# Optimization experiments

Measured on AMD Instinct MI355X. Metric: run time of the kernel, lower is better.

## Reference

```python
import jax, jax.numpy as jnp
import numpy as np

B = 8192        # number of drug-cell pairs (graphs)
NPG = 32        # nodes per graph
EPG = 64        # directed edges per graph
N = B * NPG     # total nodes
E = B * EPG     # total edges
CELL = 908      # cell_inp_dim
BN_EPS = 1e-5


def _bn(x):
    # BatchNorm1d in training mode with gamma=1, beta=0 (fresh init), biased var
    m = x.mean(0)
    v = x.var(0)
    return (x - m) * jax.lax.rsqrt(v + BN_EPS)


def _lin_params(k, fan_in, fan_out):
    kw, _ = jax.random.split(k)
    w = jax.random.normal(kw, (fan_in, fan_out), jnp.float32) / np.sqrt(fan_in)
    b = jnp.zeros((fan_out,), jnp.float32)
    return w, b


_DIMS = [("ce_1", CELL, 516), ("ce_2", 516, 256), ("ce_3", 256, 128),
         ("g1_1", 9, 128), ("g1_2", 128, 128),
         ("g2_1", 128, 128), ("g2_2", 128, 128),
         ("d_1", 128, 128), ("d_2", 128, 128),
         ("f_1", 256, 128), ("f_2", 128, 64), ("f_3", 64, 1)]


def setup_inputs() -> dict:
    key = jax.random.key(0)
    ks = jax.random.split(key, 4 + len(_DIMS))
    inp = {}
    inp["cell"] = jax.random.normal(ks[0], (B, CELL), jnp.float32)
    inp["drug_x"] = jax.random.normal(ks[1], (N, 9), jnp.float32)
    g = jnp.arange(E) // EPG  # graph id per edge
    src = g * NPG + jax.random.randint(ks[2], (E,), 0, NPG)
    dst = g * NPG + jax.random.randint(ks[3], (E,), 0, NPG)
    inp["drug_edge_index"] = jnp.stack([src, dst]).astype(jnp.int32)
    inp["drug_batch"] = (jnp.arange(N) // NPG).astype(jnp.int32)
    for i, (nm, a, b) in enumerate(_DIMS):
        w, bb = _lin_params(ks[4 + i], a, b)
        inp[nm + "_w"] = w
        inp[nm + "_b"] = bb
    return inp


def _forward(cell, drug_x, src, dst, batch,
             ce_1_w, ce_1_b, ce_2_w, ce_2_b, ce_3_w, ce_3_b,
             g1_1_w, g1_1_b, g1_2_w, g1_2_b,
             g2_1_w, g2_1_b, g2_2_w, g2_2_b,
             d_1_w, d_1_b, d_2_w, d_2_b,
             f_1_w, f_1_b, f_2_w, f_2_b, f_3_w, f_3_b):
    # cell_emb branch (dropout = identity in eval/reference)
    c = jax.nn.relu(_bn(cell @ ce_1_w + ce_1_b))
    c = jax.nn.relu(_bn(c @ ce_2_w + ce_2_b))
    c = jax.nn.relu(_bn(c @ ce_3_w + ce_3_b))

    # GINConv 1: h = MLP((1+eps)*x + sum_{j in N(i)} x_j), eps=0
    agg = jax.ops.segment_sum(drug_x[src], dst, num_segments=N)
    h = drug_x + agg
    h = jax.nn.relu(_bn(h @ g1_1_w + g1_1_b)) @ g1_2_w + g1_2_b  # inner MLP: Lin-BN-ReLU-Lin
    h = _bn(jax.nn.relu(h))  # outer ReLU then BN (per Sequential order)

    # GINConv 2
    agg = jax.ops.segment_sum(h[src], dst, num_segments=N)
    h = h + agg
    h = jax.nn.relu(_bn(h @ g2_1_w + g2_1_b)) @ g2_2_w + g2_2_b
    h = _bn(jax.nn.relu(h))

    # global max pool over nodes of each graph -> [B, 128]
    p = jax.ops.segment_max(h, batch, num_segments=B)

    d = jax.nn.relu(_bn(p @ d_1_w + d_1_b))
    d = jax.nn.relu(d @ d_2_w + d_2_b)

    z = jnp.concatenate([c, d], axis=-1)  # [B, 256]
    z = jax.nn.elu(_bn(z @ f_1_w + f_1_b))
    z = jax.nn.elu(_bn(z @ f_2_w + f_2_b))
    y = (z @ f_3_w + f_3_b).reshape(B)
    return y


def reference(cell, drug_x, drug_edge_index, drug_batch,
              ce_1_w, ce_1_b, ce_2_w, ce_2_b, ce_3_w, ce_3_b,
              g1_1_w, g1_1_b, g1_2_w, g1_2_b,
              g2_1_w, g2_1_b, g2_2_w, g2_2_b,
              d_1_w, d_1_b, d_2_w, d_2_b,
              f_1_w, f_1_b, f_2_w, f_2_b, f_3_w, f_3_b):
    src, dst = drug_edge_index[0], drug_edge_index[1]
    return _forward(cell, drug_x, src, dst, drug_batch,
                    ce_1_w, ce_1_b, ce_2_w, ce_2_b, ce_3_w, ce_3_b,
                    g1_1_w, g1_1_b, g1_2_w, g1_2_b,
                    g2_1_w, g2_1_b, g2_2_w, g2_2_b,
                    d_1_w, d_1_b, d_2_w, d_2_b,
                    f_1_w, f_1_b, f_2_w, f_2_b, f_3_w, f_3_b)
```

## Files before the change

kernel.cpp:

```cpp
#include <hip/hip_runtime.h>
#include <hip/hip_bf16.h>
#include <math.h>

#define BGRAPH 8192
#define NPG 32
#define EPG 64
#define NNODE (BGRAPH * NPG)
#define NEDGE (BGRAPH * EPG)
#define CELLD 908
#define BN_EPS 1e-5f
#define ABF_STR 960
#define C1_STR 576

typedef __attribute__((ext_vector_type(8))) short bf16x8;
typedef __attribute__((ext_vector_type(4))) float f32x4;
typedef __attribute__((ext_vector_type(4))) unsigned short us4;
typedef __attribute__((ext_vector_type(8))) unsigned short us8;

__device__ __forceinline__ unsigned short f2bf(float f)
{
    unsigned int u = __float_as_uint(f);
    u = (u + 0x7FFFu + ((u >> 16) & 1u)) >> 16;
    return (unsigned short)u;
}

__device__ __forceinline__ bf16x8 quant8(const float v[8])
{
    union { bf16x8 b; unsigned short u[8]; } fr;
    #pragma unroll
    for (int j = 0; j < 8; ++j) fr.u[j] = f2bf(v[j]);
    return fr.b;
}

__device__ __forceinline__ void bf2f8(bf16x8 b, float v[8])
{
    union { bf16x8 bb; unsigned short u[8]; } x; x.bb = b;
    #pragma unroll
    for (int j = 0; j < 8; ++j) v[j] = __uint_as_float((unsigned)x.u[j] << 16);
}

__device__ __forceinline__ float apply_in(float v, int mode, float mn, float iv)
{
    if (mode == 1)      { v = (v - mn) * iv; v = fmaxf(v, 0.f); }
    else if (mode == 2) { v = (v - mn) * iv; v = (v > 0.f) ? v : expm1f(v); }
    else if (mode == 3) { v = fmaxf(v, 0.f); v = (v - mn) * iv; }
    return v;
}

struct TransArgs {
    const float* w[11];
    unsigned short* wt[11];
    int K[11], N[11], ntN[11];
    int off[12];
};

__global__ void transpose_w(TransArgs a)
{
    __shared__ float t[64][65];
    int b = blockIdx.x, tid = threadIdx.x;
    int s = 0;
    while (s < 10 && b >= a.off[s + 1]) ++s;
    int t0 = b - a.off[s];
    int K = a.K[s], N = a.N[s], ntn = a.ntN[s];
    int kt = t0 / ntn, nt = t0 - kt * ntn;
    int k0 = kt * 64, n0 = nt * 64;
    const float* w = a.w[s];
    unsigned short* wt = a.wt[s];
    int c = tid & 63, rg = tid >> 6;
    #pragma unroll
    for (int i = 0; i < 16; ++i) {
        int rr = rg * 16 + i;
        int k = k0 + rr, n = n0 + c;
        t[c][rr] = (k < K && n < N) ? w[(size_t)k * N + n] : 0.f;
    }
    __syncthreads();
    #pragma unroll
    for (int i = 0; i < 16; ++i) {
        int rr = rg * 16 + i;
        int n = n0 + rr, k = k0 + c;
        if (n < N && k < K) wt[(size_t)n * K + k] = f2bf(t[rr][c]);
    }
}

struct SetupArgs {
    float* zb; int zTotal; int zBlocks;
    const int* src; const int* dst; int* row_start; int* col_idx;
};

__global__ void setup_all(SetupArgs a)
{
    int b = blockIdx.x;
    int tid = threadIdx.x;
    if (b < a.zBlocks) {
        int i = b * 256 + tid;
        if (i < a.zTotal) a.zb[i] = 0.f;
        return;
    }
    b -= a.zBlocks;
    __shared__ int cnt[4][32], fill[4][32], rsl[4][33];
    int gl = tid >> 6, e = tid & 63;
    int g = b * 4 + gl;
    if (e < 32) { cnt[gl][e] = 0; fill[gl][e] = 0; }
    __syncthreads();
    int s = a.src[g * EPG + e] - g * NPG;
    int d = a.dst[g * EPG + e] - g * NPG;
    atomicAdd(&cnt[gl][d], 1);
    __syncthreads();
    if (e == 0) {
        int acc = 0;
        for (int i = 0; i < 32; ++i) { rsl[gl][i] = acc; acc += cnt[gl][i]; }
        rsl[gl][32] = acc;
    }
    __syncthreads();
    int pos = rsl[gl][d] + atomicAdd(&fill[gl][d], 1);
    a.col_idx[g * EPG + pos] = s;
    if (e < 33) a.row_start[g * 33 + e] = rsl[gl][e];
}

__global__ void quant_cell(const float* __restrict__ cell, unsigned short* __restrict__ abf)
{
    int i = blockIdx.x * 256 + threadIdx.x;
    int row = i / (ABF_STR / 4), c4 = i - row * (ABF_STR / 4);
    int k = c4 * 4;
    us4 w = (us4){0, 0, 0, 0};
    if (k < CELLD) {
        float4 f = *(const float4*)&cell[(size_t)row * CELLD + k];
        w = (us4){ f2bf(f.x), f2bf(f.y), f2bf(f.z), f2bf(f.w) };
    }
    *(us4*)&abf[(size_t)row * ABF_STR + k] = w;
}

__global__ void quant_c1(const float* __restrict__ c1, const float* __restrict__ stats,
                         float inv_sM, unsigned short* __restrict__ out)
{
    int i = blockIdx.x * 256 + threadIdx.x;
    int row = i / (C1_STR / 4), c4 = i - row * (C1_STR / 4);
    int k = c4 * 4;
    us4 w = (us4){0, 0, 0, 0};
    if (k < 516) {
        float4 f = *(const float4*)&c1[(size_t)row * 516 + k];
        float v[4] = {f.x, f.y, f.z, f.w};
        #pragma unroll
        for (int j = 0; j < 4; ++j) {
            float s = stats[k + j], ss = stats[516 + k + j];
            float mn = s * inv_sM;
            float iv = rsqrtf(ss * inv_sM - mn * mn + BN_EPS);
            v[j] = fmaxf((v[j] - mn) * iv, 0.f);
        }
        w = (us4){ f2bf(v[0]), f2bf(v[1]), f2bf(v[2]), f2bf(v[3]) };
    }
    *(us4*)&out[(size_t)row * C1_STR + k] = w;
}

__global__ void reduce_stats(const float* __restrict__ part, int nrows, int nt,
                             float* __restrict__ out)
{
    int c = threadIdx.x;
    int per = nrows >> 6;
    int r0 = blockIdx.x * per;
    bool isq = (c >= 128);
    int cc = isq ? c - 128 : c;
    if (cc >= nt) return;
    float s = 0.f;
    for (int r = 0; r < per; ++r) s += part[(size_t)(r0 + r) * 256 + c];
    unsafeAtomicAdd(&out[(isq ? nt : 0) + cc], s);
}

#define HBS 136

__launch_bounds__(256)
__global__ void gin_s1(const float* __restrict__ drug_x,
                       const int* __restrict__ row_start,
                       const int* __restrict__ col_idx,
                       const unsigned short* __restrict__ W11,
                       const float* __restrict__ b11,
                       unsigned short* uout,
                       float* __restrict__ part)
{
    __shared__ __align__(16) unsigned short h[4 * 32 * HBS];
    __shared__ __align__(16) unsigned char ubuf[4096];
    __shared__ int rs[4][36];
    __shared__ int ci[4][64];

    unsigned short* w11l = (unsigned short*)ubuf;
    float* red = (float*)ubuf;

    int tid  = threadIdx.x;
    int wave = tid >> 6;
    int lane = tid & 63;
    int quad = lane >> 4;
    int l16  = lane & 15;
    int g0   = blockIdx.x * 4;
    unsigned short* hw = h + wave * (32 * HBS);
    float* xw = (float*)hw;

    for (int i = tid; i < 128 * 16; i += 256) {
        int n = i >> 4, k = i & 15;
        w11l[i] = (k < 9) ? W11[n * 9 + k] : (unsigned short)0;
    }
    if (tid < 132) {
        int gl = tid / 33, idx = tid - gl * 33;
        rs[gl][idx] = row_start[(g0 + gl) * 33 + idx];
    }
    {
        int gl = tid >> 6, e = tid & 63;
        ci[gl][e] = col_idx[(g0 + gl) * EPG + e];
    }
    {
        const float* xg = drug_x + (size_t)(g0 + wave) * 32 * 9;
        for (int i = lane; i < 32 * 16; i += 64) {
            int rr = i >> 4, c = i & 15;
            xw[i] = (c < 9) ? xg[rr * 9 + c] : 0.f;
        }
    }
    __syncthreads();

    f32x4 acc[2][8];
    #pragma unroll
    for (int i = 0; i < 2; ++i)
        #pragma unroll
        for (int j = 0; j < 8; ++j)
            acc[i][j] = (f32x4){0.f, 0.f, 0.f, 0.f};

    {
        bf16x8 af[2];
        #pragma unroll
        for (int mt = 0; mt < 2; ++mt) {
            int rowl = mt * 16 + l16;
            float v[8] = {0, 0, 0, 0, 0, 0, 0, 0};
            if (quad < 2) {
                float4 lo = *(const float4*)&xw[rowl * 16 + quad * 8];
                float4 hi = *(const float4*)&xw[rowl * 16 + quad * 8 + 4];
                v[0] = lo.x; v[1] = lo.y; v[2] = lo.z; v[3] = lo.w;
                v[4] = hi.x; v[5] = hi.y; v[6] = hi.z; v[7] = hi.w;
                int e0 = rs[wave][rowl], e1 = rs[wave][rowl + 1];
                for (int e = e0; e < e1; ++e) {
                    int sr = ci[wave][e];
                    float4 l2 = *(const float4*)&xw[sr * 16 + quad * 8];
                    float4 h2 = *(const float4*)&xw[sr * 16 + quad * 8 + 4];
                    v[0] += l2.x; v[1] += l2.y; v[2] += l2.z; v[3] += l2.w;
                    v[4] += h2.x; v[5] += h2.y; v[6] += h2.z; v[7] += h2.w;
                }
            }
            af[mt] = quant8(v);
        }
        #pragma unroll
        for (int nt = 0; nt < 8; ++nt) {
            bf16x8 b;
            if (quad < 2) b = *(const bf16x8*)(const void*)&w11l[(nt * 16 + l16) * 16 + quad * 8];
            else { float z[8] = {0,0,0,0,0,0,0,0}; b = quant8(z); }
            acc[0][nt] = __builtin_amdgcn_mfma_f32_16x16x32_bf16(af[0], b, acc[0][nt], 0, 0, 0);
            acc[1][nt] = __builtin_amdgcn_mfma_f32_16x16x32_bf16(af[1], b, acc[1][nt], 0, 0, 0);
        }
    }

    float ls[8], lq[8];
    unsigned short* ub = uout + (size_t)(g0 + wave) * 32 * 128;
    #pragma unroll
    for (int nt = 0; nt < 8; ++nt) {
        int col = nt * 16 + l16;
        float bv = b11[col];
        float s0 = 0.f, q0 = 0.f;
        #pragma unroll
        for (int mt = 0; mt < 2; ++mt) {
            int rb = mt * 16 + quad * 4;
            #pragma unroll
            for (int r = 0; r < 4; ++r) {
                float u = acc[mt][nt][r] + bv;
                ub[(size_t)(rb + r) * 128 + col] = f2bf(u);
                s0 += u; q0 += u * u;
            }
        }
        ls[nt] = s0; lq[nt] = q0;
    }
    __syncthreads();
    #pragma unroll
    for (int nt = 0; nt < 8; ++nt) {
        float s = ls[nt], q = lq[nt];
        s += __shfl_xor(s, 16); q += __shfl_xor(q, 16);
        s += __shfl_xor(s, 32); q += __shfl_xor(q, 32);
        if (quad == 0) {
            int col = nt * 16 + l16;
            red[(wave * 2 + 0) * 128 + col] = s;
            red[(wave * 2 + 1) * 128 + col] = q;
        }
    }
    __syncthreads();
    if (tid < 128) {
        float s = red[0 * 128 + tid] + red[2 * 128 + tid] + red[4 * 128 + tid] + red[6 * 128 + tid];
        float q = red[1 * 128 + tid] + red[3 * 128 + tid] + red[5 * 128 + tid] + red[7 * 128 + tid];
        part[(size_t)blockIdx.x * 256 + tid] = s;
        part[(size_t)blockIdx.x * 256 + 128 + tid] = q;
    }
}

__launch_bounds__(256)
__global__ void gin_s3f(const unsigned short* __restrict__ uin,
                        const int* __restrict__ row_start,
                        const int* __restrict__ col_idx,
                        const unsigned short* __restrict__ Wt,
                        const float* __restrict__ bias,
                        const float* __restrict__ in_stats, float inv_sM,
                        unsigned short* __restrict__ uout,
                        float* __restrict__ part)
{
    __shared__ __align__(16) unsigned short wsl[128 * 136];
    __shared__ float pmv[256];
    __shared__ int rs[2][33];
    __shared__ int ci[2][64];
    float* zt = (float*)wsl;

    int tid  = threadIdx.x;
    int wave = tid >> 6;
    int lane = tid & 63;
    int quad = lane >> 4;
    int l16  = lane & 15;
    int g0   = blockIdx.x * 2;
    int row0 = blockIdx.x * 64;

    if (tid < 128) {
        float s = in_stats[tid], ss = in_stats[128 + tid];
        float mn = s * inv_sM;
        pmv[tid] = mn;
        pmv[128 + tid] = rsqrtf(ss * inv_sM - mn * mn + BN_EPS);
    }
    if (tid < 66) {
        int gl = tid / 33, idx = tid - gl * 33;
        rs[gl][idx] = row_start[(g0 + gl) * 33 + idx];
    }
    if (tid >= 128) {
        int t = tid - 128;
        ci[t >> 6][t & 63] = col_idx[(g0 + (t >> 6)) * EPG + (t & 63)];
    }
    for (int i = tid; i < 128 * 32; i += 256) {
        int n = i >> 5, k = (i & 31) * 4;
        *(us4*)&wsl[n * 136 + k] = *(const us4*)&Wt[(size_t)n * 128 + k];
    }
    __syncthreads();

    bf16x8 afrag[4];
    {
        const unsigned short* ap = uin + (size_t)(row0 + wave * 16 + l16) * 128;
        #pragma unroll
        for (int ks = 0; ks < 4; ++ks) {
            int kb = ks * 32 + quad * 8;
            float v[8];
            bf2f8(*(const bf16x8*)(const void*)&ap[kb], v);
            #pragma unroll
            for (int j = 0; j < 8; ++j)
                v[j] = (fmaxf(v[j], 0.f) - pmv[kb + j]) * pmv[128 + kb + j];
            afrag[ks] = quant8(v);
        }
    }

    f32x4 acc[8];
    #pragma unroll
    for (int j = 0; j < 8; ++j) acc[j] = (f32x4){0.f, 0.f, 0.f, 0.f};
    #pragma unroll
    for (int ks = 0; ks < 4; ++ks) {
        int kb = ks * 32 + quad * 8;
        #pragma unroll
        for (int nt = 0; nt < 8; ++nt) {
            bf16x8 b = *(const bf16x8*)(const void*)&wsl[(nt * 16 + l16) * 136 + kb];
            acc[nt] = __builtin_amdgcn_mfma_f32_16x16x32_bf16(afrag[ks], b, acc[nt], 0, 0, 0);
        }
    }
    __syncthreads();

    #pragma unroll
    for (int nt = 0; nt < 8; ++nt) {
        int col = nt * 16 + l16;
        #pragma unroll
        for (int r = 0; r < 4; ++r)
            zt[(wave * 16 + quad * 4 + r) * 132 + col] = acc[nt][r];
    }
    __syncthreads();

    float sv[4] = {0.f, 0.f, 0.f, 0.f}, qv[4] = {0.f, 0.f, 0.f, 0.f};
    {
        int c4  = (tid & 31) * 4;
        int rg  = tid >> 5;
        int hh  = rg >> 2;
        int rb0 = (rg & 3) * 8;
        float4 bv = *(const float4*)&bias[c4];
        unsigned short* ub = uout + (size_t)row0 * 128;
        for (int rr = 0; rr < 8; ++rr) {
            int r = rb0 + rr;
            int lr = hh * 32 + r;
            float4 val = *(const float4*)&zt[lr * 132 + c4];
            int e0 = rs[hh][r], e1 = rs[hh][r + 1];
            for (int e = e0; e < e1; ++e) {
                float4 zz = *(const float4*)&zt[(hh * 32 + ci[hh][e]) * 132 + c4];
                val.x += zz.x; val.y += zz.y; val.z += zz.z; val.w += zz.w;
            }
            float u0 = val.x + bv.x, u1 = val.y + bv.y;
            float u2 = val.z + bv.z, u3 = val.w + bv.w;
            *(us4*)&ub[(size_t)lr * 128 + c4] =
                (us4){ f2bf(u0), f2bf(u1), f2bf(u2), f2bf(u3) };
            sv[0] += u0; sv[1] += u1; sv[2] += u2; sv[3] += u3;
            qv[0] += u0 * u0; qv[1] += u1 * u1; qv[2] += u2 * u2; qv[3] += u3 * u3;
        }
    }
    __syncthreads();
    {
        int c4 = (tid & 31) * 4, rg = tid >> 5;
        #pragma unroll
        for (int j = 0; j < 4; ++j) {
            zt[rg * 128 + c4 + j] = sv[j];
            zt[1024 + rg * 128 + c4 + j] = qv[j];
        }
    }
    __syncthreads();
    if (tid < 128) {
        float s = 0.f, q = 0.f;
        #pragma unroll
        for (int rg = 0; rg < 8; ++rg) {
            s += zt[rg * 128 + tid];
            q += zt[1024 + rg * 128 + tid];
        }
        part[(size_t)blockIdx.x * 256 + tid] = s;
        part[(size_t)blockIdx.x * 256 + 128 + tid] = q;
    }
}

template<int DO_POOL>
__launch_bounds__(256)
__global__ void gin_lin(const unsigned short* __restrict__ uin,
                        const unsigned short* __restrict__ Wt,
                        const float* __restrict__ bias,
                        const float* __restrict__ in_stats, float inv_sM,
                        unsigned short* uout,
                        float* __restrict__ part,
                        float* __restrict__ pool_out)
{
    __shared__ __align__(16) unsigned short Ws_l[128 * 136];
    __shared__ float pmv[256];
    __shared__ float red[4][2][128];

    int tid  = threadIdx.x;
    int wave = tid >> 6;
    int lane = tid & 63;
    int quad = lane >> 4;
    int l16  = lane & 15;
    int row0 = blockIdx.x * 64;

    for (int i = tid; i < 128 * 32; i += 256) {
        int n = i >> 5, k = (i & 31) * 4;
        *(us4*)&Ws_l[n * 136 + k] = *(const us4*)&Wt[(size_t)n * 128 + k];
    }
    if (tid < 128) {
        float s = in_stats[tid], ss = in_stats[128 + tid];
        float mn = s * inv_sM;
        pmv[tid] = mn;
        pmv[128 + tid] = rsqrtf(ss * inv_sM - mn * mn + BN_EPS);
    }
    __syncthreads();

    bf16x8 afrag[4];
    {
        const unsigned short* ap = uin + (size_t)(row0 + wave * 16 + l16) * 128;
        #pragma unroll
        for (int ks = 0; ks < 4; ++ks) {
            int kb = ks * 32 + quad * 8;
            float v[8];
            bf2f8(*(const bf16x8*)(const void*)&ap[kb], v);
            #pragma unroll
            for (int j = 0; j < 8; ++j)
                v[j] = fmaxf((v[j] - pmv[kb + j]) * pmv[128 + kb + j], 0.f);
            afrag[ks] = quant8(v);
        }
    }

    f32x4 acc[8];
    #pragma unroll
    for (int j = 0; j < 8; ++j) acc[j] = (f32x4){0.f, 0.f, 0.f, 0.f};
    #pragma unroll
    for (int ks = 0; ks < 4; ++ks) {
        int kb = ks * 32 + quad * 8;
        #pragma unroll
        for (int nt = 0; nt < 8; ++nt) {
            bf16x8 b = *(const bf16x8*)(const void*)&Ws_l[(nt * 16 + l16) * 136 + kb];
            acc[nt] = __builtin_amdgcn_mfma_f32_16x16x32_bf16(afrag[ks], b, acc[nt], 0, 0, 0);
        }
    }

    float ls[8], lq[8], lm[8];
    #pragma unroll
    for (int nt = 0; nt < 8; ++nt) {
        int col = nt * 16 + l16;
        float bv = bias[col];
        int rb = row0 + wave * 16 + quad * 4;
        float s0 = 0.f, q0 = 0.f, mx = -INFINITY;
        #pragma unroll
        for (int r = 0; r < 4; ++r) {
            float u = acc[nt][r] + bv;
            float ru = fmaxf(u, 0.f);
            s0 += ru; q0 += ru * ru;
            if (DO_POOL) mx = fmaxf(mx, ru);
            else uout[(size_t)(rb + r) * 128 + col] = f2bf(u);
        }
        ls[nt] = s0; lq[nt] = q0; lm[nt] = mx;
    }

    #pragma unroll
    for (int nt = 0; nt < 8; ++nt) {
        float s = ls[nt], q = lq[nt];
        s += __shfl_xor(s, 16); q += __shfl_xor(q, 16);
        s += __shfl_xor(s, 32); q += __shfl_xor(q, 32);
        if (quad == 0) {
            red[wave][0][nt * 16 + l16] = s;
            red[wave][1][nt * 16 + l16] = q;
        }
    }
    __syncthreads();
    if (tid < 128) {
        float s = red[0][0][tid] + red[1][0][tid] + red[2][0][tid] + red[3][0][tid];
        float q = red[0][1][tid] + red[1][1][tid] + red[2][1][tid] + red[3][1][tid];
        part[(size_t)blockIdx.x * 256 + tid] = s;
        part[(size_t)blockIdx.x * 256 + 128 + tid] = q;
    }
    if (DO_POOL) {
        __syncthreads();
        #pragma unroll
        for (int nt = 0; nt < 8; ++nt) {
            float m = lm[nt];
            m = fmaxf(m, __shfl_xor(m, 16));
            m = fmaxf(m, __shfl_xor(m, 32));
            if (quad == 0) red[wave][0][nt * 16 + l16] = m;
        }
        __syncthreads();
        {
            int gi = tid >> 7, col = tid & 127;
            float m = fmaxf(red[gi * 2][0][col], red[gi * 2 + 1][0][col]);
            pool_out[(size_t)((row0 >> 5) + gi) * 128 + col] = m;
        }
    }
}

template<int KSTEPS, int NT>
__launch_bounds__(256)
__global__ void gemm_rB(const float* __restrict__ A, const float* __restrict__ A2,
                        int lda, int K, int stats_K, int ksplit,
                        const unsigned short* __restrict__ Wt,
                        const float* __restrict__ bias, float* __restrict__ C,
                        const float* __restrict__ in_stats, float inv_sM, int in_mode,
                        float* __restrict__ part, int stats_mode, int out_act)
{
    constexpr int NSUBW = NT / 64;
    __shared__ float pm[KSTEPS * 32], pv[KSTEPS * 32];

    int tid  = threadIdx.x;
    int wave = tid >> 6;
    int lane = tid & 63;
    int quad = lane >> 4;
    int l16  = lane & 15;
    int m0   = blockIdx.x * 16;

    if (in_mode) {
        for (int k = tid; k < KSTEPS * 32; k += 256) {
            float mn = 0.f, iv = 1.f;
            if (k < stats_K) {
                float s = in_stats[k], ss = in_stats[stats_K + k];
                mn = s * inv_sM;
                float vr = ss * inv_sM - mn * mn;
                iv = rsqrtf(vr + BN_EPS);
            }
            pm[k] = mn; pv[k] = iv;
        }
        __syncthreads();
    }

    bf16x8 afrag[KSTEPS];
    {
        int row = m0 + l16;
        const float* ap = A + (size_t)row * lda;
        #pragma unroll
        for (int ks = 0; ks < KSTEPS; ++ks) {
            int kb = ks * 32 + quad * 8;
            float v[8];
            #pragma unroll
            for (int hh = 0; hh < 2; ++hh) {
                int k = kb + hh * 4;
                const float* p = (k >= ksplit) ? &A2[(size_t)row * 128 + (k - 128)]
                                               : &ap[k];
                float4 f = *(const float4*)p;
                v[hh * 4 + 0] = f.x; v[hh * 4 + 1] = f.y;
                v[hh * 4 + 2] = f.z; v[hh * 4 + 3] = f.w;
            }
            if (in_mode) {
                #pragma unroll
                for (int j = 0; j < 8; ++j)
                    v[j] = apply_in(v[j], in_mode, pm[kb + j], pv[kb + j]);
            }
            afrag[ks] = quant8(v);
        }
    }

    f32x4 acc[NSUBW];
    #pragma unroll
    for (int j = 0; j < NSUBW; ++j) acc[j] = (f32x4){0.f, 0.f, 0.f, 0.f};

    #pragma unroll
    for (int ks = 0; ks < KSTEPS; ++ks) {
        #pragma unroll
        for (int nt = 0; nt < NSUBW; ++nt) {
            int wrow = (wave * NSUBW + nt) * 16 + l16;
            bf16x8 b = *(const bf16x8*)(const void*)&Wt[(size_t)wrow * K + ks * 32 + quad * 8];
            acc[nt] = __builtin_amdgcn_mfma_f32_16x16x32_bf16(afrag[ks], b, acc[nt], 0, 0, 0);
        }
    }

    float ls[NSUBW], lq[NSUBW];
    #pragma unroll
    for (int nt = 0; nt < NSUBW; ++nt) { ls[nt] = 0.f; lq[nt] = 0.f; }

    #pragma unroll
    for (int nt = 0; nt < NSUBW; ++nt) {
        int col = (wave * NSUBW + nt) * 16 + l16;
        float bv = bias[col];
        int rbase = m0 + quad * 4;
        #pragma unroll
        for (int r = 0; r < 4; ++r) {
            float u = acc[nt][r] + bv;
            if (C) {
                float wv = out_act ? fmaxf(u, 0.f) : u;
                C[(size_t)(rbase + r) * NT + col] = wv;
            }
            if (stats_mode) {
                float s = (stats_mode == 2) ? fmaxf(u, 0.f) : u;
                ls[nt] += s; lq[nt] += s * s;
            }
        }
    }

    if (stats_mode) {
        #pragma unroll
        for (int nt = 0; nt < NSUBW; ++nt) {
            float s = ls[nt], q = lq[nt];
            s += __shfl_xor(s, 16); q += __shfl_xor(q, 16);
            s += __shfl_xor(s, 32); q += __shfl_xor(q, 32);
            if (quad == 0) {
                int col = (wave * NSUBW + nt) * 16 + l16;
                part[(size_t)blockIdx.x * 256 + col] = s;
                part[(size_t)blockIdx.x * 256 + 128 + col] = q;
            }
        }
    }
}

template<int NT, int ABF>
__launch_bounds__(256)
__global__ void gemm_cell(const float* __restrict__ A,
                          const unsigned short* __restrict__ Abf, int abf_str,
                          const unsigned short* __restrict__ Wt,
                          const float* __restrict__ bias, float* __restrict__ C,
                          int M, int K, int N,
                          const float* __restrict__ in_stats, float inv_sM, int in_mode,
                          float* __restrict__ out_stats)
{
    constexpr int NSUB = NT / 32;
    constexpr int PMSZ = ABF ? 1 : 916;
    __shared__ unsigned short As_l[32 * 72];
    __shared__ unsigned short Ws_l[NT * 72];
    __shared__ float pm[PMSZ], pv[PMSZ];
    __shared__ float red[2][2][NT];

    int tid = threadIdx.x;
    int wave = tid >> 6;
    int lane = tid & 63;
    int quad = lane >> 4;
    int l16 = lane & 15;
    int mhalf = wave & 1, nhalf = wave >> 1;
    int m0 = blockIdx.x * 32, n0 = blockIdx.y * NT;

    if (!ABF && in_mode) {
        for (int k = tid; k < K; k += 256) {
            float s = in_stats[k], ss = in_stats[K + k];
            float mn = s * inv_sM;
            float vr = ss * inv_sM - mn * mn;
            pm[k] = mn; pv[k] = rsqrtf(vr + BN_EPS);
        }
        __syncthreads();
    }

    f32x4 acc[NSUB];
    #pragma unroll
    for (int j = 0; j < NSUB; ++j) acc[j] = (f32x4){0.f, 0.f, 0.f, 0.f};

    for (int k0 = 0; k0 < K; k0 += 64) {
        if (ABF) {
            int row = tid >> 3, c8 = (tid & 7) * 8;
            us8 w = *(const us8*)&Abf[(size_t)(m0 + row) * abf_str + k0 + c8];
            *(us8*)&As_l[row * 72 + c8] = w;
        } else {
            for (int i = tid; i < 32 * 16; i += 256) {
                int row = i >> 4, f4 = i & 15;
                int k = k0 + f4 * 4;
                us4 w4 = (us4){0, 0, 0, 0};
                if (k < K) {
                    float4 f = *(const float4*)&A[(size_t)(m0 + row) * K + k];
                    if (in_mode) {
                        f.x = apply_in(f.x, in_mode, pm[k], pv[k]);
                        f.y = apply_in(f.y, in_mode, pm[k + 1], pv[k + 1]);
                        f.z = apply_in(f.z, in_mode, pm[k + 2], pv[k + 2]);
                        f.w = apply_in(f.w, in_mode, pm[k + 3], pv[k + 3]);
                    }
                    w4 = (us4){ f2bf(f.x), f2bf(f.y), f2bf(f.z), f2bf(f.w) };
                }
                *(us4*)&As_l[row * 72 + f4 * 4] = w4;
            }
        }
        for (int i = tid; i < NT * 16; i += 256) {
            int nn = i >> 4, kt = i & 15;
            int k = k0 + kt * 4;
            int gn = n0 + nn;
            us4 w4 = (us4){0, 0, 0, 0};
            if (gn < N && k < K) w4 = *(const us4*)&Wt[(size_t)gn * K + k];
            *(us4*)&Ws_l[nn * 72 + kt * 4] = w4;
        }
        __syncthreads();
        #pragma unroll
        for (int ks = 0; ks < 2; ++ks) {
            bf16x8 a = *(const bf16x8*)(const void*)&As_l[(mhalf * 16 + l16) * 72 + ks * 32 + quad * 8];
            #pragma unroll
            for (int nt = 0; nt < NSUB; ++nt) {
                bf16x8 b = *(const bf16x8*)(const void*)
                    &Ws_l[(nhalf * (NT / 2) + nt * 16 + l16) * 72 + ks * 32 + quad * 8];
                acc[nt] = __builtin_amdgcn_mfma_f32_16x16x32_bf16(a, b, acc[nt], 0, 0, 0);
            }
        }
        __syncthreads();
    }

    float ls[NSUB], lq[NSUB];
    #pragma unroll
    for (int nt = 0; nt < NSUB; ++nt) { ls[nt] = 0.f; lq[nt] = 0.f; }

    #pragma unroll
    for (int nt = 0; nt < NSUB; ++nt) {
        int col = n0 + nhalf * (NT / 2) + nt * 16 + l16;
        if (col < N) {
            float bv = bias[col];
            int rbase = m0 + mhalf * 16 + quad * 4;
            #pragma unroll
            for (int r = 0; r < 4; ++r) {
                float u = acc[nt][r] + bv;
                C[(size_t)(rbase + r) * N + col] = u;
                ls[nt] += u; lq[nt] += u * u;
            }
        }
    }

    #pragma unroll
    for (int nt = 0; nt < NSUB; ++nt) {
        float s = ls[nt], q = lq[nt];
        s += __shfl_xor(s, 16); q += __shfl_xor(q, 16);
        s += __shfl_xor(s, 32); q += __shfl_xor(q, 32);
        if (quad == 0) {
            int lc = nhalf * (NT / 2) + nt * 16 + l16;
            red[mhalf][0][lc] = s;
            red[mhalf][1][lc] = q;
        }
    }
    __syncthreads();
    if (tid < NT) {
        int col = n0 + tid;
        if (col < N) {
            float s = red[0][0][tid] + red[1][0][tid];
            float q = red[0][1][tid] + red[1][1][tid];
            unsafeAtomicAdd(&out_stats[col], s);
            unsafeAtomicAdd(&out_stats[N + col], q);
        }
    }
}

__global__ void final_dot(const float* __restrict__ u, const float* __restrict__ w,
                          const float* __restrict__ b, float* __restrict__ y,
                          const float* __restrict__ stats, float inv_sM)
{
    __shared__ float pmv[64], piv[64], sw[64];
    int tid = threadIdx.x;
    if (tid < 64) {
        float s = stats[tid], ss = stats[64 + tid];
        float mn = s * inv_sM;
        float vr = ss * inv_sM - mn * mn;
        pmv[tid] = mn;
        piv[tid] = rsqrtf(vr + BN_EPS);
        sw[tid] = w[tid];
    }
    __syncthreads();
    int i = blockIdx.x * blockDim.x + tid;
    if (i >= BGRAPH) return;
    float acc = 0.f;
    #pragma unroll
    for (int k = 0; k < 64; ++k) {
        float v = (u[(size_t)i * 64 + k] - pmv[k]) * piv[k];
        v = (v > 0.f) ? v : expm1f(v);
        acc += v * sw[k];
    }
    y[i] = acc + b[0];
}

extern "C" void kernel_launch(void* const* d_in, const int* in_sizes, int n_in,
                              void* d_out, int out_size, void* d_ws, size_t ws_size,
                              hipStream_t stream)
{
    const float* cell   = (const float*)d_in[0];
    const float* drug_x = (const float*)d_in[1];
    const int*   eidx   = (const int*)d_in[2];
    const float* ce1w = (const float*)d_in[4];  const float* ce1b = (const float*)d_in[5];
    const float* ce2w = (const float*)d_in[6];  const float* ce2b = (const float*)d_in[7];
    const float* ce3w = (const float*)d_in[8];  const float* ce3b = (const float*)d_in[9];
    const float* g11w = (const float*)d_in[10]; const float* g11b = (const float*)d_in[11];
    const float* g12w = (const float*)d_in[12]; const float* g12b = (const float*)d_in[13];
    const float* g21w = (const float*)d_in[14]; const float* g21b = (const float*)d_in[15];
    const float* g22w = (const float*)d_in[16]; const float* g22b = (const float*)d_in[17];
    const float* d1w  = (const float*)d_in[18]; const float* d1b  = (const float*)d_in[19];
    const float* d2w  = (const float*)d_in[20]; const float* d2b  = (const float*)d_in[21];
    const float* f1w  = (const float*)d_in[22]; const float* f1b  = (const float*)d_in[23];
    const float* f2w  = (const float*)d_in[24]; const float* f2b  = (const float*)d_in[25];
    const float* f3w  = (const float*)d_in[26]; const float* f3b  = (const float*)d_in[27];

    const int* src = eidx;
    const int* dst = eidx + NEDGE;
    float* out = (float*)d_out;

    const float INV_N = 1.f / (float)NNODE;
    const float INV_B = 1.f / (float)BGRAPH;
    const int KBIG = 1 << 30;

    float* ws = (float*)d_ws;
    unsigned short* ubg = (unsigned short*)ws;
    float* pbuf = ws + (size_t)NNODE * 64;
    float* sb   = pbuf + (size_t)BGRAPH * 128;
    unsigned short* wtb = (unsigned short*)(sb + 10 * 1032);
    auto ST = [&](int i) { return sb + (size_t)i * 1032; };
    float* st_u1    = ST(0);
    float* st_u2rel = ST(1);
    float* st_u3    = ST(2);
    float* st_u4rel = ST(3);
    float* st_c1    = ST(4);
    float* st_c2    = ST(5);
    float* st_c3    = ST(6);
    float* st_d1    = ST(7);
    float* st_f1    = ST(8);
    float* st_f2    = ST(9);

    float* c1    = ws;
    float* c2    = c1 + (size_t)BGRAPH * 516;
    float* c3u   = c2 + (size_t)BGRAPH * 256;
    float* dbuf  = c3u + (size_t)BGRAPH * 128;
    float* d2buf = dbuf + (size_t)BGRAPH * 128;
    float* f1o   = d2buf + (size_t)BGRAPH * 128;
    float* f2o   = f1o + (size_t)BGRAPH * 128;

    struct WDef { const float* w; int K; int N; };
    WDef wd[11] = {
        {ce1w, CELLD, 516}, {ce2w, 516, 256}, {ce3w, 256, 128},
        {g11w, 9, 128}, {g12w, 128, 128}, {g21w, 128, 128}, {g22w, 128, 128},
        {d1w, 128, 128}, {d2w, 128, 128}, {f1w, 256, 128}, {f2w, 128, 64}
    };
    TransArgs ta;
    int off = 0;
    unsigned short* wt[11];
    ta.off[0] = 0;
    for (int i = 0; i < 11; ++i) {
        wt[i] = wtb + off;
        ta.w[i] = wd[i].w; ta.wt[i] = wt[i];
        ta.K[i] = wd[i].K; ta.N[i] = wd[i].N;
        ta.ntN[i] = (wd[i].N + 63) / 64;
        ta.off[i + 1] = ta.off[i] + ((wd[i].K + 63) / 64) * ta.ntN[i];
        off += wd[i].K * wd[i].N;
    }

    SetupArgs sa;
    sa.zb = sb; sa.zTotal = 10 * 1032; sa.zBlocks = (10 * 1032 + 255) / 256;
    sa.src = src; sa.dst = dst;

    int csr_off = (off + 7) & ~7;
    int* row_start = (int*)(wtb + csr_off);
    int* col_idx   = row_start + (size_t)BGRAPH * 33;
    float* part = (float*)(col_idx + (size_t)NEDGE);
    unsigned short* Abf  = (unsigned short*)(part + (size_t)4096 * 256);
    unsigned short* C1bf = Abf + (size_t)BGRAPH * ABF_STR;
    sa.row_start = row_start; sa.col_idx = col_idx;

    transpose_w<<<ta.off[11], 256, 0, stream>>>(ta);
    setup_all<<<sa.zBlocks + BGRAPH / 4, 256, 0, stream>>>(sa);

    gin_s1<<<BGRAPH / 4, 256, 0, stream>>>(
        drug_x, row_start, col_idx, wt[3], g11b, ubg, part);
    reduce_stats<<<64, 256, 0, stream>>>(part, BGRAPH / 4, 128, st_u1);

    gin_lin<0><<<NNODE / 64, 256, 0, stream>>>(
        ubg, wt[4], g12b, st_u1, INV_N, ubg, part, nullptr);
    reduce_stats<<<64, 256, 0, stream>>>(part, NNODE / 64, 128, st_u2rel);

    gin_s3f<<<BGRAPH / 2, 256, 0, stream>>>(
        ubg, row_start, col_idx, wt[5], g21b, st_u2rel, INV_N, ubg, part);
    reduce_stats<<<64, 256, 0, stream>>>(part, BGRAPH / 2, 128, st_u3);

    gin_lin<1><<<NNODE / 64, 256, 0, stream>>>(
        ubg, wt[6], g22b, st_u3, INV_N, nullptr, part, pbuf);
    reduce_stats<<<64, 256, 0, stream>>>(part, NNODE / 64, 128, st_u4rel);

    quant_cell<<<(BGRAPH * (ABF_STR / 4)) / 256, 256, 0, stream>>>(cell, Abf);
    gemm_cell<128, 1><<<dim3(BGRAPH / 32, 5), 256, 0, stream>>>(
        nullptr, Abf, ABF_STR, wt[0], ce1b, c1, BGRAPH, CELLD, 516,
        nullptr, 0.f, 0, st_c1);
    quant_c1<<<(BGRAPH * (C1_STR / 4)) / 256, 256, 0, stream>>>(c1, st_c1, INV_B, C1bf);
    gemm_cell<64, 1><<<dim3(BGRAPH / 32, 4), 256, 0, stream>>>(
        nullptr, C1bf, C1_STR, wt[1], ce2b, c2, BGRAPH, 516, 256,
        nullptr, 0.f, 0, st_c2);
    gemm_rB<8, 128><<<BGRAPH / 16, 256, 0, stream>>>(
        c2, nullptr, 256, 256, 256, KBIG, wt[2], ce3b, c3u,
        st_c2, INV_B, 1, part, 1, 0);
    reduce_stats<<<64, 256, 0, stream>>>(part, BGRAPH / 16, 128, st_c3);

    gemm_rB<4, 128><<<BGRAPH / 16, 256, 0, stream>>>(
        pbuf, nullptr, 128, 128, 128, KBIG, wt[7], d1b, dbuf,
        st_u4rel, INV_N, 3, part, 1, 0);
    reduce_stats<<<64, 256, 0, stream>>>(part, BGRAPH / 16, 128, st_d1);
    gemm_rB<4, 128><<<BGRAPH / 16, 256, 0, stream>>>(
        dbuf, nullptr, 128, 128, 128, KBIG, wt[8], d2b, d2buf,
        st_d1, INV_B, 1, part, 0, 1);

    gemm_rB<8, 128><<<BGRAPH / 16, 256, 0, stream>>>(
        c3u, d2buf, 128, 256, 128, 128, wt[9], f1b, f1o,
        st_c3, INV_B, 1, part, 1, 0);
    reduce_stats<<<64, 256, 0, stream>>>(part, BGRAPH / 16, 128, st_f1);
    gemm_rB<4, 64><<<BGRAPH / 16, 256, 0, stream>>>(
        f1o, nullptr, 128, 128, 128, KBIG, wt[10], f2b, f2o,
        st_f1, INV_B, 2, part, 1, 0);
    reduce_stats<<<64, 256, 0, stream>>>(part, BGRAPH / 16, 64, st_f2);
    final_dot<<<BGRAPH / 256, 256, 0, stream>>>(f2o, f3w, f3b, out, st_f2, INV_B);
}
```

Measured before the change: 553.2 us.

## Register-prefetch next K chunk and widen K tile to 128 in cell GEMM

The cell-branch GEMM now stages each K chunk in registers. It loads the next 128-wide chunk of A and W from global memory while the current chunk is being multiplied, which hides global load latency behind MFMA work. The K tile doubles from 64 to 128, halving the number of barrier pairs per block, and the unused fp32-input path is removed. The padded bf16 buffers grow (strides 1024 and 640) so the last chunk reads within bounds. This adds quantization traffic in quant_cell/quant_c1, more LDS and more registers per block.

```diff
diff --git a/kernel.cpp b/kernel.cpp
--- a/kernel.cpp
+++ b/kernel.cpp
@@ -9,8 +9,8 @@
 #define NEDGE (BGRAPH * EPG)
 #define CELLD 908
 #define BN_EPS 1e-5f
-#define ABF_STR 960
-#define C1_STR 576
+#define ABF_STR 1024
+#define C1_STR 640
 
 typedef __attribute__((ext_vector_type(8))) short bf16x8;
 typedef __attribute__((ext_vector_type(4))) float f32x4;
@@ -648,21 +648,17 @@
     }
 }
 
-template<int NT, int ABF>
+template<int NT>
 __launch_bounds__(256)
-__global__ void gemm_cell(const float* __restrict__ A,
-                          const unsigned short* __restrict__ Abf, int abf_str,
+__global__ void gemm_cell(const unsigned short* __restrict__ Abf, int abf_str,
                           const unsigned short* __restrict__ Wt,
                           const float* __restrict__ bias, float* __restrict__ C,
-                          int M, int K, int N,
-                          const float* __restrict__ in_stats, float inv_sM, int in_mode,
-                          float* __restrict__ out_stats)
+                          int K, int N, float* __restrict__ out_stats)
 {
     constexpr int NSUB = NT / 32;
-    constexpr int PMSZ = ABF ? 1 : 916;
-    __shared__ unsigned short As_l[32 * 72];
-    __shared__ unsigned short Ws_l[NT * 72];
-    __shared__ float pm[PMSZ], pv[PMSZ];
+    constexpr int WITEMS = NT * 32 / 256;
+    __shared__ __align__(16) unsigned short As_l[32 * 136];
+    __shared__ __align__(16) unsigned short Ws_l[NT * 136];
     __shared__ float red[2][2][NT];
 
     int tid = threadIdx.x;
@@ -673,59 +669,62 @@
     int mhalf = wave & 1, nhalf = wave >> 1;
     int m0 = blockIdx.x * 32, n0 = blockIdx.y * NT;
 
-    if (!ABF && in_mode) {
-        for (int k = tid; k < K; k += 256) {
-            float s = in_stats[k], ss = in_stats[K + k];
-            float mn = s * inv_sM;
-            float vr = ss * inv_sM - mn * mn;
-            pm[k] = mn; pv[k] = rsqrtf(vr + BN_EPS);
-        }
-        __syncthreads();
-    }
-
-    f32x4 acc[NSUB];
-    #pragma unroll
-    for (int j = 0; j < NSUB; ++j) acc[j] = (f32x4){0.f, 0.f, 0.f, 0.f};
-
-    for (int k0 = 0; k0 < K; k0 += 64) {
-        if (ABF) {
-            int row = tid >> 3, c8 = (tid & 7) * 8;
-            us8 w = *(const us8*)&Abf[(size_t)(m0 + row) * abf_str + k0 + c8];
-            *(us8*)&As_l[row * 72 + c8] = w;
-        } else {
-            for (int i = tid; i < 32 * 16; i += 256) {
-                int row = i >> 4, f4 = i & 15;
-                int k = k0 + f4 * 4;
-                us4 w4 = (us4){0, 0, 0, 0};
-                if (k < K) {
-                    float4 f = *(const float4*)&A[(size_t)(m0 + row) * K + k];
-                    if (in_mode) {
-                        f.x = apply_in(f.x, in_mode, pm[k], pv[k]);
-                        f.y = apply_in(f.y, in_mode, pm[k + 1], pv[k + 1]);
-                        f.z = apply_in(f.z, in_mode, pm[k + 2], pv[k + 2]);
-                        f.w = apply_in(f.w, in_mode, pm[k + 3], pv[k + 3]);
-                    }
-                    w4 = (us4){ f2bf(f.x), f2bf(f.y), f2bf(f.z), f2bf(f.w) };
-                }
-                *(us4*)&As_l[row * 72 + f4 * 4] = w4;
-            }
-        }
-        for (int i = tid; i < NT * 16; i += 256) {
-            int nn = i >> 4, kt = i & 15;
+    us8 aReg[2];
+    us4 wReg[WITEMS];
+
+    auto loadA = [&](int k0) {
+        #pragma unroll
+        for (int t = 0; t < 2; ++t) {
+            int i = t * 256 + tid;
+            int row = i >> 4, c8 = (i & 15) * 8;
+            aReg[t] = *(const us8*)&Abf[(size_t)(m0 + row) * abf_str + k0 + c8];
+        }
+    };
+    auto loadW = [&](int k0) {
+        #pragma unroll
+        for (int t = 0; t < WITEMS; ++t) {
+            int i = t * 256 + tid;
+            int nn = i >> 5, kt = i & 31;
             int k = k0 + kt * 4;
             int gn = n0 + nn;
             us4 w4 = (us4){0, 0, 0, 0};
             if (gn < N && k < K) w4 = *(const us4*)&Wt[(size_t)gn * K + k];
-            *(us4*)&Ws_l[nn * 72 + kt * 4] = w4;
-        }
+            wReg[t] = w4;
+        }
+    };
+    auto storeAW = [&]() {
+        #pragma unroll
+        for (int t = 0; t < 2; ++t) {
+            int i = t * 256 + tid;
+            int row = i >> 4, c8 = (i & 15) * 8;
+            *(us8*)&As_l[row * 136 + c8] = aReg[t];
+        }
+        #pragma unroll
+        for (int t = 0; t < WITEMS; ++t) {
+            int i = t * 256 + tid;
+            int nn = i >> 5, kt = i & 31;
+            *(us4*)&Ws_l[nn * 136 + kt * 4] = wReg[t];
+        }
+    };
+
+    f32x4 acc[NSUB];
+    #pragma unroll
+    for (int j = 0; j < NSUB; ++j) acc[j] = (f32x4){0.f, 0.f, 0.f, 0.f};
+
+    int nch = (K + 127) >> 7;
+    loadA(0); loadW(0);
+    for (int c = 0; c < nch; ++c) {
+        storeAW();
+        if (c + 1 < nch) { loadA((c + 1) * 128); loadW((c + 1) * 128); }
         __syncthreads();
         #pragma unroll
-        for (int ks = 0; ks < 2; ++ks) {
-            bf16x8 a = *(const bf16x8*)(const void*)&As_l[(mhalf * 16 + l16) * 72 + ks * 32 + quad * 8];
+        for (int ks = 0; ks < 4; ++ks) {
+            bf16x8 a = *(const bf16x8*)(const void*)
+                &As_l[(mhalf * 16 + l16) * 136 + ks * 32 + quad * 8];
             #pragma unroll
             for (int nt = 0; nt < NSUB; ++nt) {
                 bf16x8 b = *(const bf16x8*)(const void*)
-                    &Ws_l[(nhalf * (NT / 2) + nt * 16 + l16) * 72 + ks * 32 + quad * 8];
+                    &Ws_l[(nhalf * (NT / 2) + nt * 16 + l16) * 136 + ks * 32 + quad * 8];
                 acc[nt] = __builtin_amdgcn_mfma_f32_16x16x32_bf16(a, b, acc[nt], 0, 0, 0);
             }
         }
@@ -905,13 +904,11 @@
     reduce_stats<<<64, 256, 0, stream>>>(part, NNODE / 64, 128, st_u4rel);
 
     quant_cell<<<(BGRAPH * (ABF_STR / 4)) / 256, 256, 0, stream>>>(cell, Abf);
-    gemm_cell<128, 1><<<dim3(BGRAPH / 32, 5), 256, 0, stream>>>(
-        nullptr, Abf, ABF_STR, wt[0], ce1b, c1, BGRAPH, CELLD, 516,
-        nullptr, 0.f, 0, st_c1);
+    gemm_cell<128><<<dim3(BGRAPH / 32, 5), 256, 0, stream>>>(
+        Abf, ABF_STR, wt[0], ce1b, c1, CELLD, 516, st_c1);
     quant_c1<<<(BGRAPH * (C1_STR / 4)) / 256, 256, 0, stream>>>(c1, st_c1, INV_B, C1bf);
-    gemm_cell<64, 1><<<dim3(BGRAPH / 32, 4), 256, 0, stream>>>(
-        nullptr, C1bf, C1_STR, wt[1], ce2b, c2, BGRAPH, 516, 256,
-        nullptr, 0.f, 0, st_c2);
+    gemm_cell<64><<<dim3(BGRAPH / 32, 4), 256, 0, stream>>>(
+        C1bf, C1_STR, wt[1], ce2b, c2, 516, 256, st_c2);
     gemm_rB<8, 128><<<BGRAPH / 16, 256, 0, stream>>>(
         c2, nullptr, 256, 256, 256, KBIG, wt[2], ce3b, c3u,
         st_c2, INV_B, 1, part, 1, 0);
```

New measurement: 525.9 us (median of 2 runs). 1.05x faster.
